# Kernel optimization log

Measured on AMD Instinct MI355X. Metric: run time of the kernel, lower is better.

Reference implementation:

```python
import jax, jax.numpy as jnp
import numpy as np

N, NFEAT, NHID, NHEADS, NCLASS, NBLOCKS = 4096, 1024, 64, 8, 8, 3
ALPHA = 0.1       # LeakyReLU negative slope
NEG = -9e15       # mask value used by pyGAT


def setup_inputs() -> dict:
    key = jax.random.key(0)
    ks = jax.random.split(key, 8)
    x = jax.random.normal(ks[0], (N, NFEAT), jnp.float32)
    # sparse-ish symmetric adjacency with self loops (0/1 int mask)
    a = (jax.random.uniform(ks[1], (N, N)) < 0.01).astype(jnp.int32)
    adj = jnp.maximum(jnp.maximum(a, a.T), jnp.eye(N, dtype=jnp.int32))
    s = 0.1
    W_heads = (jax.random.normal(ks[2], (NHEADS, NFEAT, NHID), jnp.float32) * s)
    a_heads = (jax.random.normal(ks[3], (NHEADS, 2 * NHID), jnp.float32) * s)
    W_out = (jax.random.normal(ks[4], (NHEADS * NHID, NHID), jnp.float32) * s)
    a_out = (jax.random.normal(ks[5], (2 * NHID,), jnp.float32) * s)
    W_gcn = (jax.random.normal(ks[6], (NBLOCKS, NHID, NHID), jnp.float32) * s)
    W_cls = (jax.random.normal(ks[7], (NHID, NCLASS), jnp.float32) * s)
    return dict(x=x, adj=adj, W_heads=W_heads, a_heads=a_heads,
                W_out=W_out, a_out=a_out, W_gcn=W_gcn, W_cls=W_cls)


def _gat_layer(h, mask, W, a, concat):
    # classic pyGAT dense GraphAttentionLayer (inference: dropout off)
    Wh = h @ W                      # [N, nhid]
    nh = Wh.shape[1]
    f1 = Wh @ a[:nh]                # [N]
    f2 = Wh @ a[nh:]                # [N]
    e = jax.nn.leaky_relu(f1[:, None] + f2[None, :], ALPHA)  # [N, N]
    att = jax.nn.softmax(jnp.where(mask, e, NEG), axis=1)
    hp = att @ Wh                   # [N, nhid]
    return jax.nn.elu(hp) if concat else hp


def reference(x, adj, W_heads, a_heads, W_out, a_out, W_gcn, W_cls):
    mask = adj > 0
    # multi-head GAT, concat heads (loop over small fixed head count to keep
    # peak memory at one [N,N] score matrix per step)
    heads = [_gat_layer(x, mask, W_heads[i], a_heads[i], True)
             for i in range(NHEADS)]
    h = jnp.concatenate(heads, axis=1)           # [N, nheads*nhid]
    h = _gat_layer(h, mask, W_out, a_out, False)  # [N, nhid]
    # ModifiedGCN: symmetric-normalized dense propagation, n_blocks + head
    af = adj.astype(h.dtype)
    dinv = jax.lax.rsqrt(jnp.sum(af, axis=1))
    a_norm = af * dinv[:, None] * dinv[None, :]   # D^-1/2 A D^-1/2
    for i in range(NBLOCKS):
        h = jax.nn.relu(a_norm @ (h @ W_gcn[i]))
    return a_norm @ (h @ W_cls)                   # [N, nclass]
```

## Files before the change

kernel.cpp:

```cpp
#include <hip/hip_runtime.h>
#include <hip/hip_bf16.h>
#include <math.h>

#define N_NODES 4096
#define NFEAT   1024
#define NHEADS  8
#define ALPHA   0.1f
#define MAXDEG  256

typedef short short8 __attribute__((ext_vector_type(8)));
typedef float f32x4  __attribute__((ext_vector_type(4)));

__device__ __forceinline__ ushort f2bf(float f) {
    uint b = __float_as_uint(f);
    b += 0x7FFFu + ((b >> 16) & 1u);
    return (ushort)(b >> 16);
}
__device__ __forceinline__ float bf2f(ushort u) {
    return __uint_as_float(((uint)u) << 16);
}

__global__ __launch_bounds__(64) void build_csr(const int* __restrict__ adj,
                                                ushort* __restrict__ csr,
                                                int* __restrict__ rowlen,
                                                float* __restrict__ dinv) {
    int row = blockIdx.x, lane = threadIdx.x;
    const int4* arow = (const int4*)(adj + (size_t)row * N_NODES);
    unsigned long long pre = (1ull << lane) - 1ull;
    int count = 0;
    ushort* crow = csr + (size_t)row * MAXDEG;
    for (int b = 0; b < N_NODES / 256; b++) {
        int4 v = arow[b * 64 + lane];
        unsigned long long m0 = __ballot(v.x != 0);
        unsigned long long m1 = __ballot(v.y != 0);
        unsigned long long m2 = __ballot(v.z != 0);
        unsigned long long m3 = __ballot(v.w != 0);
        int pos = count + __popcll(m0 & pre) + __popcll(m1 & pre)
                        + __popcll(m2 & pre) + __popcll(m3 & pre);
        int base = b * 256 + lane * 4;
        if (v.x) { if (pos < MAXDEG) crow[pos] = (ushort)base;       pos++; }
        if (v.y) { if (pos < MAXDEG) crow[pos] = (ushort)(base + 1); pos++; }
        if (v.z) { if (pos < MAXDEG) crow[pos] = (ushort)(base + 2); pos++; }
        if (v.w) { if (pos < MAXDEG) crow[pos] = (ushort)(base + 3); pos++; }
        count += __popcll(m0) + __popcll(m1) + __popcll(m2) + __popcll(m3);
    }
    if (lane == 0) {
        rowlen[row] = count < MAXDEG ? count : MAXDEG;
        dinv[row] = 1.0f / sqrtf((float)count);
    }
}

__global__ __launch_bounds__(256) void prep(const float* __restrict__ x,
                                            const float* __restrict__ Whd,
                                            const float* __restrict__ Wo,
                                            short* __restrict__ x3,
                                            short* __restrict__ W3,
                                            short* __restrict__ W23) {
    __shared__ float tile[64][65];
    int b = blockIdx.x, t = threadIdx.x;
    if (b < 4096) {
        size_t idx = ((size_t)b * 256 + t) * 4;
        int row = (int)(idx >> 10);
        int col = (int)(idx & 1023);
        float4 v = *(const float4*)(x + idx);
        ushort h0 = f2bf(v.x), h1 = f2bf(v.y), h2 = f2bf(v.z), h3 = f2bf(v.w);
        short4 h = make_short4((short)h0, (short)h1, (short)h2, (short)h3);
        short4 l = make_short4((short)f2bf(v.x - bf2f(h0)), (short)f2bf(v.y - bf2f(h1)),
                               (short)f2bf(v.z - bf2f(h2)), (short)f2bf(v.w - bf2f(h3)));
        short* rp = x3 + (size_t)row * 3072 + col;
        *(short4*)(rp)        = h;
        *(short4*)(rp + 1024) = l;
        *(short4*)(rp + 2048) = h;
        return;
    }
    const float* W; short* B3; int K, head, kb;
    if (b < 4096 + 128) { int id = b - 4096; W = Whd; B3 = W3;  K = 1024; head = id >> 4; kb = id & 15; }
    else                { int id = b - 4224; W = Wo;  B3 = W23; K = 512;  head = 0;       kb = id; }
    int k0 = kb * 64;
    const float* src = W + (size_t)head * K * 64 + (size_t)k0 * 64;
#pragma unroll
    for (int i = 0; i < 16; i++) {
        int lin = t + i * 256;
        int kk = lin >> 6, nn = lin & 63;
        tile[nn][kk] = src[kk * 64 + nn];
    }
    __syncthreads();
#pragma unroll
    for (int i = 0; i < 16; i++) {
        int lin = t + i * 256;
        int nn = lin >> 6, kk = lin & 63;
        float v = tile[nn][kk];
        ushort h = f2bf(v);
        ushort l = f2bf(v - bf2f(h));
        short* rp = B3 + (size_t)(head * 64 + nn) * (3 * (size_t)K) + k0 + kk;
        rp[0]     = (short)h;
        rp[K]     = (short)h;
        rp[2 * K] = (short)l;
    }
}

#define GBM 128
#define GBN 64
#define GBK 64
#define LDK 72

__global__ __launch_bounds__(256) void gemm_mfma(const short* __restrict__ A,
                                                 const short* __restrict__ B,
                                                 float* __restrict__ C,
                                                 int Kp, int ldc, int kChunk,
                                                 int cPartStride, int swz, int headmajor) {
    __shared__ __align__(16) short As[2][GBM * LDK];
    __shared__ __align__(16) short Bs[2][GBN * LDK];

    int tid = threadIdx.x, lane = tid & 63, wid = tid >> 6;
    int wr = wid >> 1, wc = wid & 1;
    int bx, by;
    if (swz) {
        int lin = blockIdx.x;
        bx = (lin & 7) * 4 + (lin >> 6);
        by = (lin >> 3) & 7;
    } else {
        bx = blockIdx.x; by = blockIdx.y;
    }
    int row0 = bx * GBM, col0 = by * GBN;
    int kbase = blockIdx.z * kChunk;
    C += (size_t)blockIdx.z * cPartStride;

    int aRow[4], aKc[4], bRow[2], bKc[2];
#pragma unroll
    for (int c = 0; c < 4; c++) { int lin = tid + c * 256; aRow[c] = lin >> 3; aKc[c] = (lin & 7) * 8; }
#pragma unroll
    for (int c = 0; c < 2; c++) { int lin = tid + c * 256; bRow[c] = lin >> 3; bKc[c] = (lin & 7) * 8; }

    short8 rA[4], rB[2];
    auto LOAD = [&](int k0) {
#pragma unroll
        for (int c = 0; c < 4; c++)
            rA[c] = *(const short8*)(A + (size_t)(row0 + aRow[c]) * Kp + kbase + k0 + aKc[c]);
#pragma unroll
        for (int c = 0; c < 2; c++)
            rB[c] = *(const short8*)(B + (size_t)(col0 + bRow[c]) * Kp + kbase + k0 + bKc[c]);
    };
    auto WRITE = [&](int buf) {
#pragma unroll
        for (int c = 0; c < 4; c++) *(short8*)&As[buf][aRow[c] * LDK + aKc[c]] = rA[c];
#pragma unroll
        for (int c = 0; c < 2; c++) *(short8*)&Bs[buf][bRow[c] * LDK + bKc[c]] = rB[c];
    };

    f32x4 acc[4][2];
#pragma unroll
    for (int m = 0; m < 4; m++)
#pragma unroll
        for (int n = 0; n < 2; n++) acc[m][n] = (f32x4){0.f, 0.f, 0.f, 0.f};

    LOAD(0);
    WRITE(0);
    __syncthreads();

    int nt = kChunk / GBK;
    for (int t = 0; t < nt; ++t) {
        int cur = t & 1;
        if (t + 1 < nt) LOAD((t + 1) * GBK);
#pragma unroll
        for (int ks = 0; ks < 2; ++ks) {
            short8 ah[4], bh[2];
            int ko = ks * 32 + (lane >> 4) * 8;
#pragma unroll
            for (int m = 0; m < 4; m++)
                ah[m] = *(const short8*)&As[cur][(wr * 64 + m * 16 + (lane & 15)) * LDK + ko];
#pragma unroll
            for (int n = 0; n < 2; n++)
                bh[n] = *(const short8*)&Bs[cur][(wc * 32 + n * 16 + (lane & 15)) * LDK + ko];
#pragma unroll
            for (int m = 0; m < 4; m++)
#pragma unroll
                for (int n = 0; n < 2; n++)
                    acc[m][n] = __builtin_amdgcn_mfma_f32_16x16x32_bf16(ah[m], bh[n], acc[m][n], 0, 0, 0);
        }
        if (t + 1 < nt) WRITE(cur ^ 1);
        __syncthreads();
    }

#pragma unroll
    for (int m = 0; m < 4; m++)
#pragma unroll
        for (int n = 0; n < 2; n++)
#pragma unroll
            for (int r = 0; r < 4; r++) {
                int rr = row0 + wr * 64 + m * 16 + (lane >> 4) * 4 + r;
                int cc = col0 + wc * 32 + n * 16 + (lane & 15);
                if (headmajor)
                    C[(size_t)(cc >> 6) * N_NODES * 64 + (size_t)rr * 64 + (cc & 63)] = acc[m][n][r];
                else
                    C[(size_t)rr * ldc + cc] = acc[m][n][r];
            }
}

__global__ __launch_bounds__(256) void compute_f1(const float* __restrict__ Whh,
                                                  const float* __restrict__ a,
                                                  float* __restrict__ f1h,
                                                  float* __restrict__ f2h) {
    int i = blockIdx.x, t = threadIdx.x, g = t >> 5, l = t & 31;
    const float* wr = Whh + ((size_t)g * N_NODES + i) * 64;
    float v0 = wr[l], v1 = wr[32 + l];
    const float* ag = a + g * 128;
    float p1 = v0 * ag[l] + v1 * ag[32 + l];
    float p2 = v0 * ag[64 + l] + v1 * ag[96 + l];
#pragma unroll
    for (int off = 16; off; off >>= 1) {
        p1 += __shfl_xor(p1, off, 32);
        p2 += __shfl_xor(p2, off, 32);
    }
    if (l == 0) {
        f1h[(size_t)g * N_NODES + i] = p1;
        f2h[(size_t)g * N_NODES + i] = p2;
    }
}

__global__ __launch_bounds__(256) void attn1(const float* __restrict__ Whh,
                                             const float* __restrict__ f1h,
                                             const float* __restrict__ f2h,
                                             const ushort* __restrict__ csr,
                                             const int* __restrict__ rowlen,
                                             short* __restrict__ hp3) {
    __shared__ float  w[4][MAXDEG];
    __shared__ ushort cols[4][MAXDEG];
    int lin = blockIdx.x;
    int h = lin & 7;
    int rq = lin >> 3;
    int wid = threadIdx.x >> 6, lane = threadIdx.x & 63;
    int i = rq * 4 + wid;
    int len = rowlen[i];
    const ushort* crow = csr + (size_t)i * MAXDEG;
    const float* f2p = f2h + (size_t)h * N_NODES;
    float f1v = f1h[(size_t)h * N_NODES + i];

    float ev[4]; int cv[4];
    float m = -1e30f;
#pragma unroll
    for (int c = 0; c < 4; c++) {
        int k = lane + c * 64;
        if (k < len) {
            int j = crow[k];
            float e = f1v + f2p[j];
            e = e > 0.f ? e : ALPHA * e;
            ev[c] = e; cv[c] = j;
            m = fmaxf(m, e);
        }
    }
#pragma unroll
    for (int off = 32; off; off >>= 1) m = fmaxf(m, __shfl_xor(m, off));
    float s = 0.f;
#pragma unroll
    for (int c = 0; c < 4; c++) {
        int k = lane + c * 64;
        if (k < len) {
            float ex = __expf(ev[c] - m);
            s += ex;
            w[wid][k] = ex;
            cols[wid][k] = (ushort)cv[c];
        }
    }
#pragma unroll
    for (int off = 32; off; off >>= 1) s += __shfl_xor(s, off);
    float sinv = 1.0f / s;

    int len8 = (len + 7) & ~7;
    if (lane < len8 - len) {
        w[wid][len + lane] = 0.f;
        cols[wid][len + lane] = 0;
    }

    int q = lane >> 4, d = lane & 15;
    const float4* base = (const float4*)(Whh + (size_t)h * (N_NODES * 64)) + d;
    float ax0 = 0.f, ay0 = 0.f, az0 = 0.f, aw0 = 0.f;
    float ax1 = 0.f, ay1 = 0.f, az1 = 0.f, aw1 = 0.f;
    for (int k = 0; k < len8; k += 8) {
        int   j0 = cols[wid][k + q];
        int   j1 = cols[wid][k + 4 + q];
        float w0 = w[wid][k + q];
        float w1 = w[wid][k + 4 + q];
        float4 v0 = base[(size_t)j0 * 16];
        float4 v1 = base[(size_t)j1 * 16];
        ax0 += w0 * v0.x; ay0 += w0 * v0.y; az0 += w0 * v0.z; aw0 += w0 * v0.w;
        ax1 += w1 * v1.x; ay1 += w1 * v1.y; az1 += w1 * v1.z; aw1 += w1 * v1.w;
    }
    float rx = ax0 + ax1, ry = ay0 + ay1, rz = az0 + az1, rw = aw0 + aw1;
#pragma unroll
    for (int off = 16; off <= 32; off <<= 1) {
        rx += __shfl_xor(rx, off);
        ry += __shfl_xor(ry, off);
        rz += __shfl_xor(rz, off);
        rw += __shfl_xor(rw, off);
    }
    if (lane < 16) {
        float v[4] = {rx * sinv, ry * sinv, rz * sinv, rw * sinv};
        short hi[4], lo[4];
#pragma unroll
        for (int c = 0; c < 4; c++) {
            float e = v[c] > 0.f ? v[c] : __expf(v[c]) - 1.f;
            ushort hh = f2bf(e);
            hi[c] = (short)hh;
            lo[c] = (short)f2bf(e - bf2f(hh));
        }
        short* rp = hp3 + (size_t)i * 1536 + h * 64 + d * 4;
        *(short4*)(rp)        = make_short4(hi[0], hi[1], hi[2], hi[3]);
        *(short4*)(rp + 512)  = make_short4(lo[0], lo[1], lo[2], lo[3]);
        *(short4*)(rp + 1024) = make_short4(hi[0], hi[1], hi[2], hi[3]);
    }
}

__global__ __launch_bounds__(256) void f2sum(const float* __restrict__ part,
                                             const float* __restrict__ a,
                                             float* __restrict__ Wh2,
                                             float* __restrict__ f1o,
                                             float* __restrict__ f2o) {
    int wid = threadIdx.x >> 6, l = threadIdx.x & 63;
    int i = blockIdx.x * 4 + wid;
    size_t o = (size_t)i * 64 + l;
    const size_t S = (size_t)N_NODES * 64;
    float v = part[o] + part[o + S] + part[o + 2 * S] + part[o + 3 * S];
    Wh2[o] = v;
    float p1 = v * a[l], p2 = v * a[64 + l];
#pragma unroll
    for (int off = 32; off; off >>= 1) {
        p1 += __shfl_xor(p1, off);
        p2 += __shfl_xor(p2, off);
    }
    if (l == 0) { f1o[i] = p1; f2o[i] = p2; }
}

__global__ __launch_bounds__(256) void attn2_g0(const float* __restrict__ Wh2,
                                                const float* __restrict__ f1o,
                                                const float* __restrict__ f2o,
                                                const ushort* __restrict__ csr,
                                                const int* __restrict__ rowlen,
                                                const float* __restrict__ W0,
                                                const float* __restrict__ dinv,
                                                float* __restrict__ t0) {
    __shared__ float  w[4][MAXDEG];
    __shared__ ushort cl[4][MAXDEG];
    __shared__ float  hrow[4][64];
    int wid = threadIdx.x >> 6, lane = threadIdx.x & 63;
    int i = blockIdx.x * 4 + wid;
    int len = rowlen[i];
    const ushort* crow = csr + (size_t)i * MAXDEG;
    float myf1 = f1o[i];

    float ev[4]; int cv[4];
    float m = -1e30f;
#pragma unroll
    for (int c = 0; c < 4; c++) {
        int k = lane + c * 64;
        if (k < len) {
            int j = crow[k];
            float e = myf1 + f2o[j];
            e = e > 0.f ? e : ALPHA * e;
            ev[c] = e; cv[c] = j;
            m = fmaxf(m, e);
        }
    }
#pragma unroll
    for (int off = 32; off; off >>= 1) m = fmaxf(m, __shfl_xor(m, off));
    float s = 0.f;
#pragma unroll
    for (int c = 0; c < 4; c++) {
        int k = lane + c * 64;
        if (k < len) {
            float ex = __expf(ev[c] - m);
            s += ex;
            w[wid][k] = ex;
            cl[wid][k] = (ushort)cv[c];
        }
    }
#pragma unroll
    for (int off = 32; off; off >>= 1) s += __shfl_xor(s, off);
    float sinv = 1.0f / s;

    int len8 = (len + 7) & ~7;
    if (lane < len8 - len) {
        w[wid][len + lane] = 0.f;
        cl[wid][len + lane] = 0;
    }

    int q = lane >> 4, d = lane & 15;
    const float4* base = (const float4*)Wh2 + d;
    float ax0 = 0.f, ay0 = 0.f, az0 = 0.f, aw0 = 0.f;
    float ax1 = 0.f, ay1 = 0.f, az1 = 0.f, aw1 = 0.f;
    for (int k = 0; k < len8; k += 8) {
        int   j0 = cl[wid][k + q];
        int   j1 = cl[wid][k + 4 + q];
        float w0 = w[wid][k + q];
        float w1 = w[wid][k + 4 + q];
        float4 v0 = base[(size_t)j0 * 16];
        float4 v1 = base[(size_t)j1 * 16];
        ax0 += w0 * v0.x; ay0 += w0 * v0.y; az0 += w0 * v0.z; aw0 += w0 * v0.w;
        ax1 += w1 * v1.x; ay1 += w1 * v1.y; az1 += w1 * v1.z; aw1 += w1 * v1.w;
    }
    float rx = ax0 + ax1, ry = ay0 + ay1, rz = az0 + az1, rw = aw0 + aw1;
#pragma unroll
    for (int off = 16; off <= 32; off <<= 1) {
        rx += __shfl_xor(rx, off);
        ry += __shfl_xor(ry, off);
        rz += __shfl_xor(rz, off);
        rw += __shfl_xor(rw, off);
    }
    if (lane < 16) {
        float4 r = make_float4(rx * sinv, ry * sinv, rz * sinv, rw * sinv);
        *(float4*)&hrow[wid][d * 4] = r;
    }

    float ox = 0.f, oy = 0.f, oz = 0.f, ow = 0.f;
#pragma unroll
    for (int it = 0; it < 16; it++) {
        int kk = q * 16 + it;
        float hv = hrow[wid][kk];
        float4 wv = *(const float4*)(W0 + kk * 64 + d * 4);
        ox += hv * wv.x; oy += hv * wv.y; oz += hv * wv.z; ow += hv * wv.w;
    }
#pragma unroll
    for (int off = 16; off <= 32; off <<= 1) {
        ox += __shfl_xor(ox, off);
        oy += __shfl_xor(oy, off);
        oz += __shfl_xor(oz, off);
        ow += __shfl_xor(ow, off);
    }
    if (lane < 16) {
        float di = dinv[i];
        *(float4*)(t0 + (size_t)i * 64 + d * 4) =
            make_float4(ox * di, oy * di, oz * di, ow * di);
    }
}

__global__ __launch_bounds__(256) void spmv_gemm(const float* __restrict__ t,
                                                 const ushort* __restrict__ csr,
                                                 const int* __restrict__ rowlen,
                                                 const float* __restrict__ W,
                                                 const float* __restrict__ dinv,
                                                 float* __restrict__ out) {
    __shared__ float hrow[4][64];
    int wid = threadIdx.x >> 6, lane = threadIdx.x & 63;
    int i = blockIdx.x * 4 + wid;
    int len = rowlen[i];
    const ushort* ci = csr + (size_t)i * MAXDEG;
    int q = lane >> 4, d = lane & 15;
    const float4* base = (const float4*)t + d;
    int len8 = (len + 7) & ~7;
    float ax0 = 0.f, ay0 = 0.f, az0 = 0.f, aw0 = 0.f;
    float ax1 = 0.f, ay1 = 0.f, az1 = 0.f, aw1 = 0.f;
    for (int k = 0; k < len8; k += 8) {
        int k0 = k + q, k1 = k + 4 + q;
        float m0 = k0 < len ? 1.f : 0.f;
        float m1 = k1 < len ? 1.f : 0.f;
        int j0 = ci[k0 < len ? k0 : 0];
        int j1 = ci[k1 < len ? k1 : 0];
        float4 v0 = base[(size_t)j0 * 16];
        float4 v1 = base[(size_t)j1 * 16];
        ax0 += m0 * v0.x; ay0 += m0 * v0.y; az0 += m0 * v0.z; aw0 += m0 * v0.w;
        ax1 += m1 * v1.x; ay1 += m1 * v1.y; az1 += m1 * v1.z; aw1 += m1 * v1.w;
    }
    float rx = ax0 + ax1, ry = ay0 + ay1, rz = az0 + az1, rw = aw0 + aw1;
#pragma unroll
    for (int off = 16; off <= 32; off <<= 1) {
        rx += __shfl_xor(rx, off);
        ry += __shfl_xor(ry, off);
        rz += __shfl_xor(rz, off);
        rw += __shfl_xor(rw, off);
    }
    float di = dinv[i];
    if (lane < 16) {
        float4 r = make_float4(fmaxf(rx * di, 0.f), fmaxf(ry * di, 0.f),
                               fmaxf(rz * di, 0.f), fmaxf(rw * di, 0.f));
        *(float4*)&hrow[wid][d * 4] = r;
    }

    float ox = 0.f, oy = 0.f, oz = 0.f, ow = 0.f;
#pragma unroll
    for (int it = 0; it < 16; it++) {
        int kk = q * 16 + it;
        float hv = hrow[wid][kk];
        float4 wv = *(const float4*)(W + kk * 64 + d * 4);
        ox += hv * wv.x; oy += hv * wv.y; oz += hv * wv.z; ow += hv * wv.w;
    }
#pragma unroll
    for (int off = 16; off <= 32; off <<= 1) {
        ox += __shfl_xor(ox, off);
        oy += __shfl_xor(oy, off);
        oz += __shfl_xor(oz, off);
        ow += __shfl_xor(ow, off);
    }
    if (lane < 16)
        *(float4*)(out + (size_t)i * 64 + d * 4) =
            make_float4(ox * di, oy * di, oz * di, ow * di);
}

__global__ __launch_bounds__(256) void spmv_cls(const float* __restrict__ t,
                                                const ushort* __restrict__ csr,
                                                const int* __restrict__ rowlen,
                                                const float* __restrict__ Wc,
                                                const float* __restrict__ dinv,
                                                float* __restrict__ t8) {
    __shared__ float hrow[4][64];
    int wid = threadIdx.x >> 6, lane = threadIdx.x & 63;
    int i = blockIdx.x * 4 + wid;
    int len = rowlen[i];
    const ushort* ci = csr + (size_t)i * MAXDEG;
    int q = lane >> 4, d = lane & 15;
    const float4* base = (const float4*)t + d;
    int len8 = (len + 7) & ~7;
    float ax0 = 0.f, ay0 = 0.f, az0 = 0.f, aw0 = 0.f;
    float ax1 = 0.f, ay1 = 0.f, az1 = 0.f, aw1 = 0.f;
    for (int k = 0; k < len8; k += 8) {
        int k0 = k + q, k1 = k + 4 + q;
        float m0 = k0 < len ? 1.f : 0.f;
        float m1 = k1 < len ? 1.f : 0.f;
        int j0 = ci[k0 < len ? k0 : 0];
        int j1 = ci[k1 < len ? k1 : 0];
        float4 v0 = base[(size_t)j0 * 16];
        float4 v1 = base[(size_t)j1 * 16];
        ax0 += m0 * v0.x; ay0 += m0 * v0.y; az0 += m0 * v0.z; aw0 += m0 * v0.w;
        ax1 += m1 * v1.x; ay1 += m1 * v1.y; az1 += m1 * v1.z; aw1 += m1 * v1.w;
    }
    float rx = ax0 + ax1, ry = ay0 + ay1, rz = az0 + az1, rw = aw0 + aw1;
#pragma unroll
    for (int off = 16; off <= 32; off <<= 1) {
        rx += __shfl_xor(rx, off);
        ry += __shfl_xor(ry, off);
        rz += __shfl_xor(rz, off);
        rw += __shfl_xor(rw, off);
    }
    float di = dinv[i];
    if (lane < 16) {
        float4 r = make_float4(fmaxf(rx * di, 0.f), fmaxf(ry * di, 0.f),
                               fmaxf(rz * di, 0.f), fmaxf(rw * di, 0.f));
        *(float4*)&hrow[wid][d * 4] = r;
    }
    int col = lane & 7, k0s = (lane >> 3) * 8;
    float o = 0.f;
#pragma unroll
    for (int kk = 0; kk < 8; kk++) o += hrow[wid][k0s + kk] * Wc[(k0s + kk) * 8 + col];
    o += __shfl_down(o, 32);
    o += __shfl_down(o, 16);
    o += __shfl_down(o, 8);
    if (lane < 8) t8[(size_t)i * 8 + lane] = o * di;
}

__global__ __launch_bounds__(256) void spmv8(const float* __restrict__ t8,
                                             const ushort* __restrict__ csr,
                                             const int* __restrict__ rowlen,
                                             const float* __restrict__ dinv,
                                             float* __restrict__ out) {
    int wid = threadIdx.x >> 6, lane = threadIdx.x & 63;
    int i = blockIdx.x * 4 + wid;
    int len = rowlen[i];
    const ushort* ci = csr + (size_t)i * MAXDEG;
    int col = lane & 7, chunk = lane >> 3;
    float acc = 0.f;
    for (int k = chunk; k < len; k += 8)
        acc += t8[(size_t)ci[k] * 8 + col];
    acc += __shfl_down(acc, 32);
    acc += __shfl_down(acc, 16);
    acc += __shfl_down(acc, 8);
    if (lane < 8) out[(size_t)i * 8 + lane] = acc * dinv[i];
}

extern "C" void kernel_launch(void* const* d_in, const int* in_sizes, int n_in,
                              void* d_out, int out_size, void* d_ws, size_t ws_size,
                              hipStream_t stream) {
    const float* x       = (const float*)d_in[0];
    const int*   adj     = (const int*)d_in[1];
    const float* W_heads = (const float*)d_in[2];
    const float* a_heads = (const float*)d_in[3];
    const float* W_out   = (const float*)d_in[4];
    const float* a_out   = (const float*)d_in[5];
    const float* W_gcn   = (const float*)d_in[6];
    const float* W_cls   = (const float*)d_in[7];
    float* outp = (float*)d_out;

    char* p = (char*)d_ws;
    short*  x3     = (short*)p;  p += (size_t)N_NODES * 3072 * 2;
    short*  W3     = (short*)p;  p += (size_t)512 * 3072 * 2;
    short*  W23    = (short*)p;  p += (size_t)64 * 1536 * 2;
    float*  Whh    = (float*)p;  p += (size_t)NHEADS * N_NODES * 64 * 4;
    float*  f1h    = (float*)p;  p += (size_t)NHEADS * N_NODES * 4;
    float*  f2h    = (float*)p;  p += (size_t)NHEADS * N_NODES * 4;
    float*  Wh2    = (float*)p;  p += (size_t)N_NODES * 64 * 4;
    float*  f1o    = (float*)p;  p += (size_t)N_NODES * 4;
    float*  f2o    = (float*)p;  p += (size_t)N_NODES * 4;
    float*  tA     = (float*)p;  p += (size_t)N_NODES * 64 * 4;
    float*  tB     = (float*)p;  p += (size_t)N_NODES * 64 * 4;
    float*  t8     = (float*)p;  p += (size_t)N_NODES * 8 * 4;
    float*  dinv   = (float*)p;  p += (size_t)N_NODES * 4;
    int*    rowlen = (int*)p;    p += (size_t)N_NODES * 4;
    ushort* csr    = (ushort*)p; p += (size_t)N_NODES * MAXDEG * 2;

    short* hp3  = x3;
    float* part = (float*)((char*)x3 + (16u << 20));

    build_csr<<<N_NODES, 64, 0, stream>>>(adj, csr, rowlen, dinv);

    prep<<<4096 + 128 + 8, 256, 0, stream>>>(x, W_heads, W_out, x3, W3, W23);

    gemm_mfma<<<256, 256, 0, stream>>>(x3, W3, Whh, 3072, 512, 3072, 0, 1, 1);

    compute_f1<<<N_NODES, 256, 0, stream>>>(Whh, a_heads, f1h, f2h);

    attn1<<<N_NODES * NHEADS / 4, 256, 0, stream>>>(Whh, f1h, f2h, csr, rowlen, hp3);

    gemm_mfma<<<dim3(N_NODES / GBM, 1, 4), 256, 0, stream>>>(
        hp3, W23, part, 1536, 64, 384, N_NODES * 64, 0, 0);

    f2sum<<<N_NODES / 4, 256, 0, stream>>>(part, a_out, Wh2, f1o, f2o);

    attn2_g0<<<N_NODES / 4, 256, 0, stream>>>(Wh2, f1o, f2o, csr, rowlen, W_gcn, dinv, tA);

    spmv_gemm<<<N_NODES / 4, 256, 0, stream>>>(tA, csr, rowlen, W_gcn + 4096, dinv, tB);
    spmv_gemm<<<N_NODES / 4, 256, 0, stream>>>(tB, csr, rowlen, W_gcn + 8192, dinv, tA);

    spmv_cls<<<N_NODES / 4, 256, 0, stream>>>(tA, csr, rowlen, W_cls, dinv, t8);
    spmv8<<<N_NODES / 4, 256, 0, stream>>>(t8, csr, rowlen, dinv, outp);
}
```

Before: 257.7 us.

## Merge CSR build into prep, fuse f1/f2 into GEMM epilogue, retile GEMM, unroll gathers

The CSR build and the bf16 split-precision prep now run as one kernel launch, with four adjacency rows handled per 256-thread block. The attention-score projections f1/f2 are computed in the first GEMM's epilogue, so the separate compute_f1 pass and its re-read of Whh go away. The GEMM tile shrinks from 128x64 to 64x64, doubling the block count for better CU coverage, and gets an occupancy hint. The sparse gather loops are unrolled to 16 neighbours per iteration for more memory-level parallelism, with occupancy launch bounds added.

```diff
diff --git a/kernel.cpp b/kernel.cpp
--- a/kernel.cpp
+++ b/kernel.cpp
@@ -20,42 +20,16 @@
     return __uint_as_float(((uint)u) << 16);
 }
 
-__global__ __launch_bounds__(64) void build_csr(const int* __restrict__ adj,
+__global__ __launch_bounds__(256) void prep_all(const float* __restrict__ x,
+                                                const int* __restrict__ adj,
+                                                const float* __restrict__ Whd,
+                                                const float* __restrict__ Wo,
+                                                short* __restrict__ x3,
+                                                short* __restrict__ W3,
+                                                short* __restrict__ W23,
                                                 ushort* __restrict__ csr,
                                                 int* __restrict__ rowlen,
                                                 float* __restrict__ dinv) {
-    int row = blockIdx.x, lane = threadIdx.x;
-    const int4* arow = (const int4*)(adj + (size_t)row * N_NODES);
-    unsigned long long pre = (1ull << lane) - 1ull;
-    int count = 0;
-    ushort* crow = csr + (size_t)row * MAXDEG;
-    for (int b = 0; b < N_NODES / 256; b++) {
-        int4 v = arow[b * 64 + lane];
-        unsigned long long m0 = __ballot(v.x != 0);
-        unsigned long long m1 = __ballot(v.y != 0);
-        unsigned long long m2 = __ballot(v.z != 0);
-        unsigned long long m3 = __ballot(v.w != 0);
-        int pos = count + __popcll(m0 & pre) + __popcll(m1 & pre)
-                        + __popcll(m2 & pre) + __popcll(m3 & pre);
-        int base = b * 256 + lane * 4;
-        if (v.x) { if (pos < MAXDEG) crow[pos] = (ushort)base;       pos++; }
-        if (v.y) { if (pos < MAXDEG) crow[pos] = (ushort)(base + 1); pos++; }
-        if (v.z) { if (pos < MAXDEG) crow[pos] = (ushort)(base + 2); pos++; }
-        if (v.w) { if (pos < MAXDEG) crow[pos] = (ushort)(base + 3); pos++; }
-        count += __popcll(m0) + __popcll(m1) + __popcll(m2) + __popcll(m3);
-    }
-    if (lane == 0) {
-        rowlen[row] = count < MAXDEG ? count : MAXDEG;
-        dinv[row] = 1.0f / sqrtf((float)count);
-    }
-}
-
-__global__ __launch_bounds__(256) void prep(const float* __restrict__ x,
-                                            const float* __restrict__ Whd,
-                                            const float* __restrict__ Wo,
-                                            short* __restrict__ x3,
-                                            short* __restrict__ W3,
-                                            short* __restrict__ W23) {
     __shared__ float tile[64][65];
     int b = blockIdx.x, t = threadIdx.x;
     if (b < 4096) {
@@ -73,42 +47,73 @@
         *(short4*)(rp + 2048) = h;
         return;
     }
-    const float* W; short* B3; int K, head, kb;
-    if (b < 4096 + 128) { int id = b - 4096; W = Whd; B3 = W3;  K = 1024; head = id >> 4; kb = id & 15; }
-    else                { int id = b - 4224; W = Wo;  B3 = W23; K = 512;  head = 0;       kb = id; }
-    int k0 = kb * 64;
-    const float* src = W + (size_t)head * K * 64 + (size_t)k0 * 64;
-#pragma unroll
-    for (int i = 0; i < 16; i++) {
-        int lin = t + i * 256;
-        int kk = lin >> 6, nn = lin & 63;
-        tile[nn][kk] = src[kk * 64 + nn];
-    }
-    __syncthreads();
-#pragma unroll
-    for (int i = 0; i < 16; i++) {
-        int lin = t + i * 256;
-        int nn = lin >> 6, kk = lin & 63;
-        float v = tile[nn][kk];
-        ushort h = f2bf(v);
-        ushort l = f2bf(v - bf2f(h));
-        short* rp = B3 + (size_t)(head * 64 + nn) * (3 * (size_t)K) + k0 + kk;
-        rp[0]     = (short)h;
-        rp[K]     = (short)h;
-        rp[2 * K] = (short)l;
-    }
-}
-
-#define GBM 128
+    if (b < 4232) {
+        const float* W; short* B3; int K, head, kb;
+        if (b < 4224) { int id = b - 4096; W = Whd; B3 = W3;  K = 1024; head = id >> 4; kb = id & 15; }
+        else          { int id = b - 4224; W = Wo;  B3 = W23; K = 512;  head = 0;       kb = id; }
+        int k0 = kb * 64;
+        const float* src = W + (size_t)head * K * 64 + (size_t)k0 * 64;
+#pragma unroll
+        for (int i = 0; i < 16; i++) {
+            int lin = t + i * 256;
+            int kk = lin >> 6, nn = lin & 63;
+            tile[nn][kk] = src[kk * 64 + nn];
+        }
+        __syncthreads();
+#pragma unroll
+        for (int i = 0; i < 16; i++) {
+            int lin = t + i * 256;
+            int nn = lin >> 6, kk = lin & 63;
+            float v = tile[nn][kk];
+            ushort h = f2bf(v);
+            ushort l = f2bf(v - bf2f(h));
+            short* rp = B3 + (size_t)(head * 64 + nn) * (3 * (size_t)K) + k0 + kk;
+            rp[0]     = (short)h;
+            rp[K]     = (short)h;
+            rp[2 * K] = (short)l;
+        }
+        return;
+    }
+    int wid = t >> 6, lane = t & 63;
+    int row = (b - 4232) * 4 + wid;
+    const int4* arow = (const int4*)(adj + (size_t)row * N_NODES);
+    unsigned long long pre = (1ull << lane) - 1ull;
+    int count = 0;
+    ushort* crow = csr + (size_t)row * MAXDEG;
+    for (int blk = 0; blk < N_NODES / 256; blk++) {
+        int4 v = arow[blk * 64 + lane];
+        unsigned long long m0 = __ballot(v.x != 0);
+        unsigned long long m1 = __ballot(v.y != 0);
+        unsigned long long m2 = __ballot(v.z != 0);
+        unsigned long long m3 = __ballot(v.w != 0);
+        int pos = count + __popcll(m0 & pre) + __popcll(m1 & pre)
+                        + __popcll(m2 & pre) + __popcll(m3 & pre);
+        int base = blk * 256 + lane * 4;
+        if (v.x) { if (pos < MAXDEG) crow[pos] = (ushort)base;       pos++; }
+        if (v.y) { if (pos < MAXDEG) crow[pos] = (ushort)(base + 1); pos++; }
+        if (v.z) { if (pos < MAXDEG) crow[pos] = (ushort)(base + 2); pos++; }
+        if (v.w) { if (pos < MAXDEG) crow[pos] = (ushort)(base + 3); pos++; }
+        count += __popcll(m0) + __popcll(m1) + __popcll(m2) + __popcll(m3);
+    }
+    if (lane == 0) {
+        rowlen[row] = count < MAXDEG ? count : MAXDEG;
+        dinv[row] = 1.0f / sqrtf((float)count);
+    }
+}
+
+#define GBM 64
 #define GBN 64
 #define GBK 64
 #define LDK 72
 
-__global__ __launch_bounds__(256) void gemm_mfma(const short* __restrict__ A,
-                                                 const short* __restrict__ B,
-                                                 float* __restrict__ C,
-                                                 int Kp, int ldc, int kChunk,
-                                                 int cPartStride, int swz, int headmajor) {
+__global__ __launch_bounds__(256, 2) void gemm_mfma(const short* __restrict__ A,
+                                                    const short* __restrict__ B,
+                                                    float* __restrict__ C,
+                                                    int Kp, int kChunk, int cPartStride,
+                                                    int swz, int headmajor,
+                                                    const float* __restrict__ aH,
+                                                    float* __restrict__ f1h,
+                                                    float* __restrict__ f2h) {
     __shared__ __align__(16) short As[2][GBM * LDK];
     __shared__ __align__(16) short Bs[2][GBN * LDK];
 
@@ -117,7 +122,7 @@
     int bx, by;
     if (swz) {
         int lin = blockIdx.x;
-        bx = (lin & 7) * 4 + (lin >> 6);
+        bx = (lin & 7) * 8 + (lin >> 6);
         by = (lin >> 3) & 7;
     } else {
         bx = blockIdx.x; by = blockIdx.y;
@@ -126,31 +131,33 @@
     int kbase = blockIdx.z * kChunk;
     C += (size_t)blockIdx.z * cPartStride;
 
-    int aRow[4], aKc[4], bRow[2], bKc[2];
-#pragma unroll
-    for (int c = 0; c < 4; c++) { int lin = tid + c * 256; aRow[c] = lin >> 3; aKc[c] = (lin & 7) * 8; }
-#pragma unroll
-    for (int c = 0; c < 2; c++) { int lin = tid + c * 256; bRow[c] = lin >> 3; bKc[c] = (lin & 7) * 8; }
-
-    short8 rA[4], rB[2];
+    int aRow[2], aKc[2], bRow[2], bKc[2];
+#pragma unroll
+    for (int c = 0; c < 2; c++) {
+        int lin = tid + c * 256;
+        aRow[c] = lin >> 3; aKc[c] = (lin & 7) * 8;
+        bRow[c] = lin >> 3; bKc[c] = (lin & 7) * 8;
+    }
+
+    short8 rA[2], rB[2];
     auto LOAD = [&](int k0) {
 #pragma unroll
-        for (int c = 0; c < 4; c++)
+        for (int c = 0; c < 2; c++) {
             rA[c] = *(const short8*)(A + (size_t)(row0 + aRow[c]) * Kp + kbase + k0 + aKc[c]);
-#pragma unroll
-        for (int c = 0; c < 2; c++)
             rB[c] = *(const short8*)(B + (size_t)(col0 + bRow[c]) * Kp + kbase + k0 + bKc[c]);
+        }
     };
     auto WRITE = [&](int buf) {
 #pragma unroll
-        for (int c = 0; c < 4; c++) *(short8*)&As[buf][aRow[c] * LDK + aKc[c]] = rA[c];
-#pragma unroll
-        for (int c = 0; c < 2; c++) *(short8*)&Bs[buf][bRow[c] * LDK + bKc[c]] = rB[c];
+        for (int c = 0; c < 2; c++) {
+            *(short8*)&As[buf][aRow[c] * LDK + aKc[c]] = rA[c];
+            *(short8*)&Bs[buf][bRow[c] * LDK + bKc[c]] = rB[c];
+        }
     };
 
-    f32x4 acc[4][2];
-#pragma unroll
-    for (int m = 0; m < 4; m++)
+    f32x4 acc[2][2];
+#pragma unroll
+    for (int m = 0; m < 2; m++)
 #pragma unroll
         for (int n = 0; n < 2; n++) acc[m][n] = (f32x4){0.f, 0.f, 0.f, 0.f};
 
@@ -164,16 +171,16 @@
         if (t + 1 < nt) LOAD((t + 1) * GBK);
 #pragma unroll
         for (int ks = 0; ks < 2; ++ks) {
-            short8 ah[4], bh[2];
+            short8 ah[2], bh[2];
             int ko = ks * 32 + (lane >> 4) * 8;
 #pragma unroll
-            for (int m = 0; m < 4; m++)
-                ah[m] = *(const short8*)&As[cur][(wr * 64 + m * 16 + (lane & 15)) * LDK + ko];
+            for (int m = 0; m < 2; m++)
+                ah[m] = *(const short8*)&As[cur][(wr * 32 + m * 16 + (lane & 15)) * LDK + ko];
 #pragma unroll
             for (int n = 0; n < 2; n++)
                 bh[n] = *(const short8*)&Bs[cur][(wc * 32 + n * 16 + (lane & 15)) * LDK + ko];
 #pragma unroll
-            for (int m = 0; m < 4; m++)
+            for (int m = 0; m < 2; m++)
 #pragma unroll
                 for (int n = 0; n < 2; n++)
                     acc[m][n] = __builtin_amdgcn_mfma_f32_16x16x32_bf16(ah[m], bh[n], acc[m][n], 0, 0, 0);
@@ -183,47 +190,56 @@
     }
 
 #pragma unroll
-    for (int m = 0; m < 4; m++)
+    for (int m = 0; m < 2; m++)
 #pragma unroll
         for (int n = 0; n < 2; n++)
 #pragma unroll
             for (int r = 0; r < 4; r++) {
-                int rr = row0 + wr * 64 + m * 16 + (lane >> 4) * 4 + r;
+                int rr = row0 + wr * 32 + m * 16 + (lane >> 4) * 4 + r;
                 int cc = col0 + wc * 32 + n * 16 + (lane & 15);
                 if (headmajor)
-                    C[(size_t)(cc >> 6) * N_NODES * 64 + (size_t)rr * 64 + (cc & 63)] = acc[m][n][r];
+                    C[(size_t)(cc >> 6) * (N_NODES * 64) + (size_t)rr * 64 + (cc & 63)] = acc[m][n][r];
                 else
-                    C[(size_t)rr * ldc + cc] = acc[m][n][r];
+                    C[(size_t)rr * 64 + cc] = acc[m][n][r];
             }
-}
-
-__global__ __launch_bounds__(256) void compute_f1(const float* __restrict__ Whh,
-                                                  const float* __restrict__ a,
-                                                  float* __restrict__ f1h,
-                                                  float* __restrict__ f2h) {
-    int i = blockIdx.x, t = threadIdx.x, g = t >> 5, l = t & 31;
-    const float* wr = Whh + ((size_t)g * N_NODES + i) * 64;
-    float v0 = wr[l], v1 = wr[32 + l];
-    const float* ag = a + g * 128;
-    float p1 = v0 * ag[l] + v1 * ag[32 + l];
-    float p2 = v0 * ag[64 + l] + v1 * ag[96 + l];
-#pragma unroll
-    for (int off = 16; off; off >>= 1) {
-        p1 += __shfl_xor(p1, off, 32);
-        p2 += __shfl_xor(p2, off, 32);
-    }
-    if (l == 0) {
-        f1h[(size_t)g * N_NODES + i] = p1;
-        f2h[(size_t)g * N_NODES + i] = p2;
-    }
-}
-
-__global__ __launch_bounds__(256) void attn1(const float* __restrict__ Whh,
-                                             const float* __restrict__ f1h,
-                                             const float* __restrict__ f2h,
-                                             const ushort* __restrict__ csr,
-                                             const int* __restrict__ rowlen,
-                                             short* __restrict__ hp3) {
+
+    if (aH) {
+        __shared__ float f1p[2][64], f2p[2][64];
+        const float* ahp = aH + by * 128;
+        int cl = lane & 15;
+        float a1x = ahp[wc * 32 + cl],      a1y = ahp[wc * 32 + 16 + cl];
+        float a2x = ahp[64 + wc * 32 + cl], a2y = ahp[64 + wc * 32 + 16 + cl];
+#pragma unroll
+        for (int m = 0; m < 2; m++)
+#pragma unroll
+            for (int r = 0; r < 4; r++) {
+                float s1 = acc[m][0][r] * a1x + acc[m][1][r] * a1y;
+                float s2 = acc[m][0][r] * a2x + acc[m][1][r] * a2y;
+#pragma unroll
+                for (int off = 1; off < 16; off <<= 1) {
+                    s1 += __shfl_xor(s1, off);
+                    s2 += __shfl_xor(s2, off);
+                }
+                if ((lane & 15) == 0) {
+                    int rl = wr * 32 + m * 16 + (lane >> 4) * 4 + r;
+                    f1p[wc][rl] = s1;
+                    f2p[wc][rl] = s2;
+                }
+            }
+        __syncthreads();
+        if (tid < 64) {
+            f1h[(size_t)by * N_NODES + row0 + tid] = f1p[0][tid] + f1p[1][tid];
+            f2h[(size_t)by * N_NODES + row0 + tid] = f2p[0][tid] + f2p[1][tid];
+        }
+    }
+}
+
+__global__ __launch_bounds__(256, 4) void attn1(const float* __restrict__ Whh,
+                                                const float* __restrict__ f1h,
+                                                const float* __restrict__ f2h,
+                                                const ushort* __restrict__ csr,
+                                                const int* __restrict__ rowlen,
+                                                short* __restrict__ hp3) {
     __shared__ float  w[4][MAXDEG];
     __shared__ ushort cols[4][MAXDEG];
     int lin = blockIdx.x;
@@ -266,27 +282,33 @@
     for (int off = 32; off; off >>= 1) s += __shfl_xor(s, off);
     float sinv = 1.0f / s;
 
-    int len8 = (len + 7) & ~7;
-    if (lane < len8 - len) {
+    int len16 = (len + 15) & ~15;
+    if (lane < len16 - len) {
         w[wid][len + lane] = 0.f;
         cols[wid][len + lane] = 0;
     }
 
     int q = lane >> 4, d = lane & 15;
     const float4* base = (const float4*)(Whh + (size_t)h * (N_NODES * 64)) + d;
-    float ax0 = 0.f, ay0 = 0.f, az0 = 0.f, aw0 = 0.f;
-    float ax1 = 0.f, ay1 = 0.f, az1 = 0.f, aw1 = 0.f;
-    for (int k = 0; k < len8; k += 8) {
-        int   j0 = cols[wid][k + q];
-        int   j1 = cols[wid][k + 4 + q];
-        float w0 = w[wid][k + q];
-        float w1 = w[wid][k + 4 + q];
+    f32x4 A0 = {0.f,0.f,0.f,0.f}, A1 = A0, A2 = A0, A3 = A0;
+    for (int k = 0; k < len16; k += 16) {
+        int   j0 = cols[wid][k + q];       float w0 = w[wid][k + q];
+        int   j1 = cols[wid][k + 4 + q];   float w1 = w[wid][k + 4 + q];
+        int   j2 = cols[wid][k + 8 + q];   float w2 = w[wid][k + 8 + q];
+        int   j3 = cols[wid][k + 12 + q];  float w3 = w[wid][k + 12 + q];
         float4 v0 = base[(size_t)j0 * 16];
         float4 v1 = base[(size_t)j1 * 16];
-        ax0 += w0 * v0.x; ay0 += w0 * v0.y; az0 += w0 * v0.z; aw0 += w0 * v0.w;
-        ax1 += w1 * v1.x; ay1 += w1 * v1.y; az1 += w1 * v1.z; aw1 += w1 * v1.w;
-    }
-    float rx = ax0 + ax1, ry = ay0 + ay1, rz = az0 + az1, rw = aw0 + aw1;
+        float4 v2 = base[(size_t)j2 * 16];
+        float4 v3 = base[(size_t)j3 * 16];
+        A0[0] += w0 * v0.x; A0[1] += w0 * v0.y; A0[2] += w0 * v0.z; A0[3] += w0 * v0.w;
+        A1[0] += w1 * v1.x; A1[1] += w1 * v1.y; A1[2] += w1 * v1.z; A1[3] += w1 * v1.w;
+        A2[0] += w2 * v2.x; A2[1] += w2 * v2.y; A2[2] += w2 * v2.z; A2[3] += w2 * v2.w;
+        A3[0] += w3 * v3.x; A3[1] += w3 * v3.y; A3[2] += w3 * v3.z; A3[3] += w3 * v3.w;
+    }
+    float rx = (A0[0] + A1[0]) + (A2[0] + A3[0]);
+    float ry = (A0[1] + A1[1]) + (A2[1] + A3[1]);
+    float rz = (A0[2] + A1[2]) + (A2[2] + A3[2]);
+    float rw = (A0[3] + A1[3]) + (A2[3] + A3[3]);
 #pragma unroll
     for (int off = 16; off <= 32; off <<= 1) {
         rx += __shfl_xor(rx, off);
@@ -331,14 +353,14 @@
     if (l == 0) { f1o[i] = p1; f2o[i] = p2; }
 }
 
-__global__ __launch_bounds__(256) void attn2_g0(const float* __restrict__ Wh2,
-                                                const float* __restrict__ f1o,
-                                                const float* __restrict__ f2o,
-                                                const ushort* __restrict__ csr,
-                                                const int* __restrict__ rowlen,
-                                                const float* __restrict__ W0,
-                                                const float* __restrict__ dinv,
-                                                float* __restrict__ t0) {
+__global__ __launch_bounds__(256, 4) void attn2_g0(const float* __restrict__ Wh2,
+                                                   const float* __restrict__ f1o,
+                                                   const float* __restrict__ f2o,
+                                                   const ushort* __restrict__ csr,
+                                                   const int* __restrict__ rowlen,
+                                                   const float* __restrict__ W0,
+                                                   const float* __restrict__ dinv,
+                                                   float* __restrict__ t0) {
     __shared__ float  w[4][MAXDEG];
     __shared__ ushort cl[4][MAXDEG];
     __shared__ float  hrow[4][64];
@@ -378,27 +400,33 @@
     for (int off = 32; off; off >>= 1) s += __shfl_xor(s, off);
     float sinv = 1.0f / s;
 
-    int len8 = (len + 7) & ~7;
-    if (lane < len8 - len) {
+    int len16 = (len + 15) & ~15;
+    if (lane < len16 - len) {
         w[wid][len + lane] = 0.f;
         cl[wid][len + lane] = 0;
     }
 
     int q = lane >> 4, d = lane & 15;
     const float4* base = (const float4*)Wh2 + d;
-    float ax0 = 0.f, ay0 = 0.f, az0 = 0.f, aw0 = 0.f;
-    float ax1 = 0.f, ay1 = 0.f, az1 = 0.f, aw1 = 0.f;
-    for (int k = 0; k < len8; k += 8) {
-        int   j0 = cl[wid][k + q];
-        int   j1 = cl[wid][k + 4 + q];
-        float w0 = w[wid][k + q];
-        float w1 = w[wid][k + 4 + q];
+    f32x4 A0 = {0.f,0.f,0.f,0.f}, A1 = A0, A2 = A0, A3 = A0;
+    for (int k = 0; k < len16; k += 16) {
+        int   j0 = cl[wid][k + q];       float w0 = w[wid][k + q];
+        int   j1 = cl[wid][k + 4 + q];   float w1 = w[wid][k + 4 + q];
+        int   j2 = cl[wid][k + 8 + q];   float w2 = w[wid][k + 8 + q];
+        int   j3 = cl[wid][k + 12 + q];  float w3 = w[wid][k + 12 + q];
         float4 v0 = base[(size_t)j0 * 16];
         float4 v1 = base[(size_t)j1 * 16];
-        ax0 += w0 * v0.x; ay0 += w0 * v0.y; az0 += w0 * v0.z; aw0 += w0 * v0.w;
-        ax1 += w1 * v1.x; ay1 += w1 * v1.y; az1 += w1 * v1.z; aw1 += w1 * v1.w;
-    }
-    float rx = ax0 + ax1, ry = ay0 + ay1, rz = az0 + az1, rw = aw0 + aw1;
+        float4 v2 = base[(size_t)j2 * 16];
+        float4 v3 = base[(size_t)j3 * 16];
+        A0[0] += w0 * v0.x; A0[1] += w0 * v0.y; A0[2] += w0 * v0.z; A0[3] += w0 * v0.w;
+        A1[0] += w1 * v1.x; A1[1] += w1 * v1.y; A1[2] += w1 * v1.z; A1[3] += w1 * v1.w;
+        A2[0] += w2 * v2.x; A2[1] += w2 * v2.y; A2[2] += w2 * v2.z; A2[3] += w2 * v2.w;
+        A3[0] += w3 * v3.x; A3[1] += w3 * v3.y; A3[2] += w3 * v3.z; A3[3] += w3 * v3.w;
+    }
+    float rx = (A0[0] + A1[0]) + (A2[0] + A3[0]);
+    float ry = (A0[1] + A1[1]) + (A2[1] + A3[1]);
+    float rz = (A0[2] + A1[2]) + (A2[2] + A3[2]);
+    float rw = (A0[3] + A1[3]) + (A2[3] + A3[3]);
 #pragma unroll
     for (int off = 16; off <= 32; off <<= 1) {
         rx += __shfl_xor(rx, off);
@@ -433,12 +461,12 @@
     }
 }
 
-__global__ __launch_bounds__(256) void spmv_gemm(const float* __restrict__ t,
-                                                 const ushort* __restrict__ csr,
-                                                 const int* __restrict__ rowlen,
-                                                 const float* __restrict__ W,
-                                                 const float* __restrict__ dinv,
-                                                 float* __restrict__ out) {
+__global__ __launch_bounds__(256, 4) void spmv_gemm(const float* __restrict__ t,
+                                                    const ushort* __restrict__ csr,
+                                                    const int* __restrict__ rowlen,
+                                                    const float* __restrict__ W,
+                                                    const float* __restrict__ dinv,
+                                                    float* __restrict__ out) {
     __shared__ float hrow[4][64];
     int wid = threadIdx.x >> 6, lane = threadIdx.x & 63;
     int i = blockIdx.x * 4 + wid;
@@ -446,21 +474,31 @@
     const ushort* ci = csr + (size_t)i * MAXDEG;
     int q = lane >> 4, d = lane & 15;
     const float4* base = (const float4*)t + d;
-    int len8 = (len + 7) & ~7;
-    float ax0 = 0.f, ay0 = 0.f, az0 = 0.f, aw0 = 0.f;
-    float ax1 = 0.f, ay1 = 0.f, az1 = 0.f, aw1 = 0.f;
-    for (int k = 0; k < len8; k += 8) {
-        int k0 = k + q, k1 = k + 4 + q;
+    int len16 = (len + 15) & ~15;
+    f32x4 A0 = {0.f,0.f,0.f,0.f}, A1 = A0, A2 = A0, A3 = A0;
+    for (int k = 0; k < len16; k += 16) {
+        int k0 = k + q, k1 = k + 4 + q, k2 = k + 8 + q, k3 = k + 12 + q;
         float m0 = k0 < len ? 1.f : 0.f;
         float m1 = k1 < len ? 1.f : 0.f;
+        float m2 = k2 < len ? 1.f : 0.f;
+        float m3 = k3 < len ? 1.f : 0.f;
         int j0 = ci[k0 < len ? k0 : 0];
         int j1 = ci[k1 < len ? k1 : 0];
+        int j2 = ci[k2 < len ? k2 : 0];
+        int j3 = ci[k3 < len ? k3 : 0];
         float4 v0 = base[(size_t)j0 * 16];
         float4 v1 = base[(size_t)j1 * 16];
-        ax0 += m0 * v0.x; ay0 += m0 * v0.y; az0 += m0 * v0.z; aw0 += m0 * v0.w;
-        ax1 += m1 * v1.x; ay1 += m1 * v1.y; az1 += m1 * v1.z; aw1 += m1 * v1.w;
-    }
-    float rx = ax0 + ax1, ry = ay0 + ay1, rz = az0 + az1, rw = aw0 + aw1;
+        float4 v2 = base[(size_t)j2 * 16];
+        float4 v3 = base[(size_t)j3 * 16];
+        A0[0] += m0 * v0.x; A0[1] += m0 * v0.y; A0[2] += m0 * v0.z; A0[3] += m0 * v0.w;
+        A1[0] += m1 * v1.x; A1[1] += m1 * v1.y; A1[2] += m1 * v1.z; A1[3] += m1 * v1.w;
+        A2[0] += m2 * v2.x; A2[1] += m2 * v2.y; A2[2] += m2 * v2.z; A2[3] += m2 * v2.w;
+        A3[0] += m3 * v3.x; A3[1] += m3 * v3.y; A3[2] += m3 * v3.z; A3[3] += m3 * v3.w;
+    }
+    float rx = (A0[0] + A1[0]) + (A2[0] + A3[0]);
+    float ry = (A0[1] + A1[1]) + (A2[1] + A3[1]);
+    float rz = (A0[2] + A1[2]) + (A2[2] + A3[2]);
+    float rw = (A0[3] + A1[3]) + (A2[3] + A3[3]);
 #pragma unroll
     for (int off = 16; off <= 32; off <<= 1) {
         rx += __shfl_xor(rx, off);
@@ -495,12 +533,12 @@
             make_float4(ox * di, oy * di, oz * di, ow * di);
 }
 
-__global__ __launch_bounds__(256) void spmv_cls(const float* __restrict__ t,
-                                                const ushort* __restrict__ csr,
-                                                const int* __restrict__ rowlen,
-                                                const float* __restrict__ Wc,
-                                                const float* __restrict__ dinv,
-                                                float* __restrict__ t8) {
+__global__ __launch_bounds__(256, 4) void spmv_cls(const float* __restrict__ t,
+                                                   const ushort* __restrict__ csr,
+                                                   const int* __restrict__ rowlen,
+                                                   const float* __restrict__ Wc,
+                                                   const float* __restrict__ dinv,
+                                                   float* __restrict__ t8) {
     __shared__ float hrow[4][64];
     int wid = threadIdx.x >> 6, lane = threadIdx.x & 63;
     int i = blockIdx.x * 4 + wid;
@@ -508,21 +546,31 @@
     const ushort* ci = csr + (size_t)i * MAXDEG;
     int q = lane >> 4, d = lane & 15;
     const float4* base = (const float4*)t + d;
-    int len8 = (len + 7) & ~7;
-    float ax0 = 0.f, ay0 = 0.f, az0 = 0.f, aw0 = 0.f;
-    float ax1 = 0.f, ay1 = 0.f, az1 = 0.f, aw1 = 0.f;
-    for (int k = 0; k < len8; k += 8) {
-        int k0 = k + q, k1 = k + 4 + q;
+    int len16 = (len + 15) & ~15;
+    f32x4 A0 = {0.f,0.f,0.f,0.f}, A1 = A0, A2 = A0, A3 = A0;
+    for (int k = 0; k < len16; k += 16) {
+        int k0 = k + q, k1 = k + 4 + q, k2 = k + 8 + q, k3 = k + 12 + q;
         float m0 = k0 < len ? 1.f : 0.f;
         float m1 = k1 < len ? 1.f : 0.f;
+        float m2 = k2 < len ? 1.f : 0.f;
+        float m3 = k3 < len ? 1.f : 0.f;
         int j0 = ci[k0 < len ? k0 : 0];
         int j1 = ci[k1 < len ? k1 : 0];
+        int j2 = ci[k2 < len ? k2 : 0];
+        int j3 = ci[k3 < len ? k3 : 0];
         float4 v0 = base[(size_t)j0 * 16];
         float4 v1 = base[(size_t)j1 * 16];
-        ax0 += m0 * v0.x; ay0 += m0 * v0.y; az0 += m0 * v0.z; aw0 += m0 * v0.w;
-        ax1 += m1 * v1.x; ay1 += m1 * v1.y; az1 += m1 * v1.z; aw1 += m1 * v1.w;
-    }
-    float rx = ax0 + ax1, ry = ay0 + ay1, rz = az0 + az1, rw = aw0 + aw1;
+        float4 v2 = base[(size_t)j2 * 16];
+        float4 v3 = base[(size_t)j3 * 16];
+        A0[0] += m0 * v0.x; A0[1] += m0 * v0.y; A0[2] += m0 * v0.z; A0[3] += m0 * v0.w;
+        A1[0] += m1 * v1.x; A1[1] += m1 * v1.y; A1[2] += m1 * v1.z; A1[3] += m1 * v1.w;
+        A2[0] += m2 * v2.x; A2[1] += m2 * v2.y; A2[2] += m2 * v2.z; A2[3] += m2 * v2.w;
+        A3[0] += m3 * v3.x; A3[1] += m3 * v3.y; A3[2] += m3 * v3.z; A3[3] += m3 * v3.w;
+    }
+    float rx = (A0[0] + A1[0]) + (A2[0] + A3[0]);
+    float ry = (A0[1] + A1[1]) + (A2[1] + A3[1]);
+    float rz = (A0[2] + A1[2]) + (A2[2] + A3[2]);
+    float rw = (A0[3] + A1[3]) + (A2[3] + A3[3]);
 #pragma unroll
     for (int off = 16; off <= 32; off <<= 1) {
         rx += __shfl_xor(rx, off);
@@ -598,18 +646,16 @@
     short* hp3  = x3;
     float* part = (float*)((char*)x3 + (16u << 20));
 
-    build_csr<<<N_NODES, 64, 0, stream>>>(adj, csr, rowlen, dinv);
-
-    prep<<<4096 + 128 + 8, 256, 0, stream>>>(x, W_heads, W_out, x3, W3, W23);
-
-    gemm_mfma<<<256, 256, 0, stream>>>(x3, W3, Whh, 3072, 512, 3072, 0, 1, 1);
-
-    compute_f1<<<N_NODES, 256, 0, stream>>>(Whh, a_heads, f1h, f2h);
+    prep_all<<<4096 + 128 + 8 + 1024, 256, 0, stream>>>(
+        x, adj, W_heads, W_out, x3, W3, W23, csr, rowlen, dinv);
+
+    gemm_mfma<<<512, 256, 0, stream>>>(x3, W3, Whh, 3072, 3072, 0, 1, 1,
+                                       a_heads, f1h, f2h);
 
     attn1<<<N_NODES * NHEADS / 4, 256, 0, stream>>>(Whh, f1h, f2h, csr, rowlen, hp3);
 
     gemm_mfma<<<dim3(N_NODES / GBM, 1, 4), 256, 0, stream>>>(
-        hp3, W23, part, 1536, 64, 384, N_NODES * 64, 0, 0);
+        hp3, W23, part, 1536, 384, N_NODES * 64, 0, 0, nullptr, nullptr, nullptr);
 
     f2sum<<<N_NODES / 4, 256, 0, stream>>>(part, a_out, Wh2, f1o, f2o);
 
```

Measured after the change: 244.1 us. 1.06x faster.
